# Optimization experiments

Measured on AMD Instinct MI355X. Metric: run time of the kernel, lower is better.

Reference implementation:

```python
import math
import jax, jax.numpy as jnp
import numpy as np

B, S, D, H, V = 8, 1024, 512, 8, 32000
HD = D // H


def _position_embedding(seq_len, d_model):
    pos = jnp.arange(seq_len, dtype=jnp.float32)[:, None]                 # [S,1]
    div = jnp.exp(jnp.arange(0, d_model, 2, dtype=jnp.float32) * (-math.log(10000.0) / d_model))  # [D/2]
    ang = pos * div                                                        # [S,D/2]
    # interleave sin (even cols) / cos (odd cols)
    return jnp.stack([jnp.sin(ang), jnp.cos(ang)], axis=-1).reshape(seq_len, d_model)


def _min_max_normalize(w):
    lo = jnp.min(w, axis=-1, keepdims=True)
    hi = jnp.max(w, axis=-1, keepdims=True)
    return (w - lo) / (hi - lo)


def _converable_mask(h, Wc, bc):
    bs, seq = h.shape[0], h.shape[1]
    half = seq // 2
    shift = math.ceil(seq / 2)
    width = jnp.einsum('bsd,od->bso', h, Wc)[..., 0] + bc[0]               # [B,S]
    width = _min_max_normalize(width)[..., None]                           # [B,S,1]
    origin = jnp.concatenate([jnp.linspace(1.0, 0.0, half),
                              jnp.linspace(0.0, 1.0, seq - half)])         # [S]
    origin_mask = 1.0 - jax.nn.sigmoid((origin[None, None, :] - width) * 100.0)  # [B,S,S]
    idx = (jnp.arange(seq - 1, -1, -1)[:, None] + jnp.arange(seq)[None, :]) % seq  # [S,S]
    idx = jnp.roll(idx, shift, axis=0)
    # torch.roll of a [1,S] row along dim 0 is a no-op
    cmp = idx >= jnp.arange(seq)[None, :]                                  # [S,S] bool
    move = jnp.concatenate([cmp[:shift], ~cmp[shift:]], axis=0)            # [S,S]
    gathered = jnp.take_along_axis(origin_mask, idx[None, :, :], axis=2)   # [B,S,S]
    return gathered * move.astype(origin_mask.dtype)


def setup_inputs():
    key = jax.random.key(0)
    ks = jax.random.split(key, 9)
    s_emb = 1.0
    s_hd = 1.0 / math.sqrt(HD)
    s_d = 1.0 / math.sqrt(D)
    return {
        'x':   jax.random.randint(ks[0], (B, S), 0, V),
        'emb': jax.random.normal(ks[1], (V, D), dtype=jnp.float32) * s_emb,
        'Wq':  jax.random.normal(ks[2], (HD, HD), dtype=jnp.float32) * s_hd,
        'Wk':  jax.random.normal(ks[3], (HD, HD), dtype=jnp.float32) * s_hd,
        'Wv':  jax.random.normal(ks[4], (HD, HD), dtype=jnp.float32) * s_hd,
        'Wo':  jax.random.normal(ks[5], (D, D), dtype=jnp.float32) * s_d,
        'bo':  jnp.zeros((D,), dtype=jnp.float32),
        'Wc':  jax.random.normal(ks[6], (1, D), dtype=jnp.float32) * s_d,
        'bc':  jnp.zeros((1,), dtype=jnp.float32),
    }


def reference(x, emb, Wq, Wk, Wv, Wo, bo, Wc, bc):
    h = emb[x] + _position_embedding(S, D)[None]                           # [B,S,D]
    mask = _converable_mask(h, Wc, bc)                                     # [B,S,S]
    hh = h.reshape(B, S, H, HD)
    q = jnp.einsum('bshd,od->bsho', hh, Wq)
    k = jnp.einsum('bshd,od->bsho', hh, Wk)
    v = jnp.einsum('bshd,od->bsho', hh, Wv)
    energy = jnp.einsum('bqhd,bkhd->bhqk', q, k)                           # [B,H,S,S]
    # mask [B,S,S] broadcasts as [1,B,S,S]; valid because B == H (as in original)
    energy = energy * mask
    attn = jax.nn.softmax(energy / math.sqrt(D), axis=3)
    out = jnp.einsum('bhqk,bkhd->bqhd', attn, v).reshape(B, S, D)
    out = out @ Wo.T + bo
    return (out, mask)
```

## Files before the change

kernel.cpp:

```cpp
#include <hip/hip_runtime.h>
#include <hip/hip_bf16.h>
#include <math.h>

#define Bn 8
#define Sn 1024
#define Dn 512
#define Hn 8
#define HDn 64

typedef __bf16 bf16x8 __attribute__((ext_vector_type(8)));
typedef __bf16 bf16x4 __attribute__((ext_vector_type(4)));
typedef __bf16 bf16x2 __attribute__((ext_vector_type(2)));
typedef float  f32x4  __attribute__((ext_vector_type(4)));
typedef float  f32x16 __attribute__((ext_vector_type(16)));
typedef unsigned int u32x4 __attribute__((ext_vector_type(4)));
typedef int i32x2 __attribute__((ext_vector_type(2)));

__device__ __forceinline__ unsigned enc_f(float v) {
    unsigned u = __float_as_uint(v);
    return (u & 0x80000000u) ? ~u : (u | 0x80000000u);
}
__device__ __forceinline__ float dec_f(unsigned k) {
    unsigned u = (k & 0x80000000u) ? (k ^ 0x80000000u) : ~k;
    return __uint_as_float(u);
}

__global__ __launch_bounds__(256) void k_fused(
        const int* __restrict__ x, const float* __restrict__ emb,
        const float* __restrict__ Wc, const float* __restrict__ bc,
        const float* __restrict__ Wq, const float* __restrict__ Wk,
        const float* __restrict__ Wv,
        float* __restrict__ width, unsigned* __restrict__ lohi,
        __bf16* __restrict__ q, __bf16* __restrict__ k, __bf16* __restrict__ vt) {
    __shared__ __align__(16) __bf16 Xs[64][72];
    __shared__ __align__(16) __bf16 WqS[64][72];
    __shared__ __align__(16) __bf16 WkS[64][72];
    __shared__ __align__(16) __bf16 WvS[64][72];
    __shared__ float wtok[8];
    int t = threadIdx.x;
    int bs0 = blockIdx.x * 8;
    int m0 = blockIdx.x * 64;
    int w = t >> 6, lane = t & 63, quad = lane >> 4, li = lane & 15;

    {
        int token = t >> 5, l32 = t & 31;
        int bs = bs0 + token;
        int s = bs & (Sn - 1);
        int tok = x[bs];
        float wpart = 0.f;
        int row = token * 8 + ((l32 * 16) >> 6);
        #pragma unroll
        for (int j = 0; j < 4; ++j) {
            int d0 = l32 * 16 + j * 4;
            float4 ev = *(const float4*)&emb[(size_t)tok * Dn + d0];
            float4 wc = *(const float4*)&Wc[d0];
            float hv[4];
            #pragma unroll
            for (int i = 0; i < 4; ++i) {
                int d = d0 + i;
                float f = __expf((float)(d & ~1) * (-9.210340371976184f / 512.0f));
                float ang = (float)s * f;
                float pe = (d & 1) ? __cosf(ang) : __sinf(ang);
                hv[i] = (&ev.x)[i] + pe;
                wpart += hv[i] * (&wc.x)[i];
            }
            *(bf16x4*)&Xs[row][d0 & 63] =
                (bf16x4){(__bf16)hv[0], (__bf16)hv[1], (__bf16)hv[2], (__bf16)hv[3]};
        }
        #pragma unroll
        for (int off = 1; off < 32; off <<= 1) wpart += __shfl_xor(wpart, off);
        if (l32 == 0) { float wv = wpart + bc[0]; width[bs] = wv; wtok[token] = wv; }
    }
    #pragma unroll
    for (int it = 0; it < 4; ++it) {
        int e = (it * 256 + t) * 4; int r = e >> 6, c = e & 63;
        float4 qv = *(const float4*)&Wq[e];
        *(bf16x4*)&WqS[r][c] = (bf16x4){(__bf16)qv.x, (__bf16)qv.y, (__bf16)qv.z, (__bf16)qv.w};
        float4 kv = *(const float4*)&Wk[e];
        *(bf16x4*)&WkS[r][c] = (bf16x4){(__bf16)kv.x, (__bf16)kv.y, (__bf16)kv.z, (__bf16)kv.w};
        float4 vv = *(const float4*)&Wv[e];
        *(bf16x4*)&WvS[r][c] = (bf16x4){(__bf16)vv.x, (__bf16)vv.y, (__bf16)vv.z, (__bf16)vv.w};
    }
    __syncthreads();

    if (t == 0) {
        float mn = wtok[0], mx = wtok[0];
        #pragma unroll
        for (int i = 1; i < 8; ++i) { mn = fminf(mn, wtok[i]); mx = fmaxf(mx, wtok[i]); }
        int b = bs0 >> 10;
        atomicMin(&lohi[b], enc_f(mn));
        atomicMin(&lohi[8 + b], ~enc_f(mx));
    }

    bf16x8 A0 = *(const bf16x8*)&Xs[w * 16 + li][quad * 8];
    bf16x8 A1 = *(const bf16x8*)&Xs[w * 16 + li][32 + quad * 8];
    f32x4 aq[4], ak[4], av[4];
    #pragma unroll
    for (int n = 0; n < 4; ++n) {
        aq[n] = (f32x4){0.f,0.f,0.f,0.f}; ak[n] = aq[n]; av[n] = aq[n];
        bf16x8 Bq0 = *(const bf16x8*)&WqS[n * 16 + li][quad * 8];
        bf16x8 Bq1 = *(const bf16x8*)&WqS[n * 16 + li][32 + quad * 8];
        aq[n] = __builtin_amdgcn_mfma_f32_16x16x32_bf16(A0, Bq0, aq[n], 0, 0, 0);
        aq[n] = __builtin_amdgcn_mfma_f32_16x16x32_bf16(A1, Bq1, aq[n], 0, 0, 0);
        bf16x8 Bk0 = *(const bf16x8*)&WkS[n * 16 + li][quad * 8];
        bf16x8 Bk1 = *(const bf16x8*)&WkS[n * 16 + li][32 + quad * 8];
        ak[n] = __builtin_amdgcn_mfma_f32_16x16x32_bf16(A0, Bk0, ak[n], 0, 0, 0);
        ak[n] = __builtin_amdgcn_mfma_f32_16x16x32_bf16(A1, Bk1, ak[n], 0, 0, 0);
        bf16x8 Bv0 = *(const bf16x8*)&WvS[n * 16 + li][quad * 8];
        bf16x8 Bv1 = *(const bf16x8*)&WvS[n * 16 + li][32 + quad * 8];
        av[n] = __builtin_amdgcn_mfma_f32_16x16x32_bf16(A0, Bv0, av[n], 0, 0, 0);
        av[n] = __builtin_amdgcn_mfma_f32_16x16x32_bf16(A1, Bv1, av[n], 0, 0, 0);
    }

    const float SCALE = 0.04419417382415922f;
    __syncthreads();
    #pragma unroll
    for (int n = 0; n < 4; ++n)
        #pragma unroll
        for (int r = 0; r < 4; ++r) {
            int row = w * 16 + quad * 4 + r, col = n * 16 + li;
            WkS[row][col] = (__bf16)(aq[n][r] * SCALE);
            WvS[row][col] = (__bf16)ak[n][r];
            WqS[row][col] = (__bf16)av[n][r];
        }
    __syncthreads();

    {
        int row = t >> 2, part = (t & 3) * 16;
        int Rg = m0 + row;
        int bsI = Rg >> 3, head = Rg & 7;
        int bq = bsI >> 10, sq = bsI & (Sn - 1);
        size_t base = (((size_t)(bq * Hn + head)) * Sn + sq) * HDn + part;
        *(bf16x8*)&q[base]     = *(bf16x8*)&WkS[row][part];
        *(bf16x8*)&q[base + 8] = *(bf16x8*)&WkS[row][part + 8];
        *(bf16x8*)&k[base]     = *(bf16x8*)&WvS[row][part];
        *(bf16x8*)&k[base + 8] = *(bf16x8*)&WvS[row][part + 8];
    }

    __bf16 (*Vs)[72] = WqS;
    int bs0i = m0 >> 3;
    int b = bs0i >> 10, s0l = bs0i & (Sn - 1);
    #pragma unroll
    for (int i = 0; i < 2; ++i) {
        int p = t + 256 * i;
        int head = p >> 6, o = p & 63;
        __bf16 tmp[8];
        #pragma unroll
        for (int j = 0; j < 8; ++j) tmp[j] = Vs[j * 8 + head][o];
        *(bf16x8*)&vt[(((size_t)(b * Hn + head)) * HDn + o) * Sn + s0l] = *(bf16x8*)tmp;
    }
}

__global__ void k_mask(const float* __restrict__ width, const unsigned* __restrict__ lohi,
                       float* __restrict__ mask_out, __bf16* __restrict__ maskb) {
    int bs = blockIdx.x;
    int b = bs >> 10;
    int s = bs & (Sn - 1);
    float lo = dec_f(lohi[b]);
    float hi = dec_f(~lohi[8 + b]);
    float wn = (width[bs] - lo) / (hi - lo);
    for (int t = threadIdx.x; t < Sn; t += 256) {
        int it = (t - s + 1535) & (Sn - 1);
        float origin = (it < 512) ? (1.0f - (float)it * (1.0f / 511.0f))
                                  : ((float)(it - 512) * (1.0f / 511.0f));
        float z = (origin - wn) * 100.0f;
        float om;
        if (z >= 0.0f) { float e = __expf(-z); om = e / (1.0f + e); }
        else           { float e = __expf(z);  om = 1.0f / (1.0f + e); }
        bool cmpv = (it >= t);
        bool mv = (s < 512) ? cmpv : !cmpv;
        float val = mv ? om : 0.0f;
        mask_out[(size_t)bs * Sn + t] = val;
        maskb[(size_t)bs * Sn + t] = (__bf16)val;
    }
}

__global__ __launch_bounds__(256, 2) void k_attn(
        const __bf16* __restrict__ q, const __bf16* __restrict__ k,
        const __bf16* __restrict__ vt, const __bf16* __restrict__ maskb,
        __bf16* __restrict__ ao) {
    __shared__ __align__(16) __bf16 Ks[2][64][72];
    __shared__ __align__(16) __bf16 Vt[2][64][72];
    int blk = blockIdx.x;
    int hh = blk & 7;
    int qt = (blk >> 3) & 7;
    int b  = blk >> 6;
    int bh = b * Hn + hh;
    int q0 = qt * 128;
    int t = threadIdx.x;
    int w = t >> 6, lane = t & 63, hi5 = lane >> 5, l31 = lane & 31;

    const __bf16* qbase  = q  + ((size_t)bh * Sn + q0 + w * 32) * HDn;
    const __bf16* kbase  = k  + (size_t)bh * Sn * HDn;
    const __bf16* vtbase = vt + (size_t)bh * HDn * Sn;
    const __bf16* mq = maskb + ((size_t)hh * Sn + q0 + w * 32 + l31) * Sn;

    bf16x8 Qf[4];
    #pragma unroll
    for (int c = 0; c < 4; ++c)
        Qf[c] = *(const bf16x8*)&qbase[(size_t)l31 * HDn + c * 16 + hi5 * 8];

    int sr0 = t >> 3, sc0 = (t & 7) * 8;
    bf16x8 pk0, pk1, pv0, pv1;
    pk0 = *(const bf16x8*)&kbase[(size_t)sr0 * HDn + sc0];
    pk1 = *(const bf16x8*)&kbase[(size_t)(sr0 + 32) * HDn + sc0];
    pv0 = *(const bf16x8*)&vtbase[(size_t)sr0 * Sn + sc0];
    pv1 = *(const bf16x8*)&vtbase[(size_t)(sr0 + 32) * Sn + sc0];
    *(bf16x8*)&Ks[0][sr0][sc0] = pk0;
    *(bf16x8*)&Ks[0][sr0 + 32][sc0] = pk1;
    *(bf16x8*)&Vt[0][sr0][sc0] = pv0;
    *(bf16x8*)&Vt[0][sr0 + 32][sc0] = pv1;

    bf16x4 mc[2][4];
    #pragma unroll
    for (int kg = 0; kg < 2; ++kg)
        #pragma unroll
        for (int g = 0; g < 4; ++g)
            mc[kg][g] = *(const bf16x4*)&mq[kg * 32 + g * 8 + hi5 * 4];

    __syncthreads();

    f32x16 OT[2];
    OT[0] = (f32x16){0.f,0.f,0.f,0.f,0.f,0.f,0.f,0.f,0.f,0.f,0.f,0.f,0.f,0.f,0.f,0.f};
    OT[1] = OT[0];
    float rs = 0.f;

    for (int ti = 0; ti < 16; ++ti) {
        int cur = ti & 1;

        bf16x4 mn_[2][4];
        if (ti < 15) {
            int k0n = (ti + 1) * 64;
            #pragma unroll
            for (int kg = 0; kg < 2; ++kg)
                #pragma unroll
                for (int g = 0; g < 4; ++g)
                    mn_[kg][g] = *(const bf16x4*)&mq[k0n + kg * 32 + g * 8 + hi5 * 4];
            pk0 = *(const bf16x8*)&kbase[(size_t)(k0n + sr0) * HDn + sc0];
            pk1 = *(const bf16x8*)&kbase[(size_t)(k0n + sr0 + 32) * HDn + sc0];
            pv0 = *(const bf16x8*)&vtbase[(size_t)sr0 * Sn + k0n + sc0];
            pv1 = *(const bf16x8*)&vtbase[(size_t)(sr0 + 32) * Sn + k0n + sc0];
        }

        bf16x8 Kf[2][4], Vf[2][4];
        #pragma unroll
        for (int h = 0; h < 2; ++h)
            #pragma unroll
            for (int c = 0; c < 4; ++c)
                Kf[h][c] = *(const bf16x8*)&Ks[cur][h * 32 + l31][c * 16 + hi5 * 8];
        #pragma unroll
        for (int h = 0; h < 2; ++h)
            #pragma unroll
            for (int c = 0; c < 4; ++c)
                Vf[h][c] = *(const bf16x8*)&Vt[cur][h * 32 + l31][c * 16 + hi5 * 8];

        f32x16 St[2];
        St[0] = (f32x16){0.f,0.f,0.f,0.f,0.f,0.f,0.f,0.f,0.f,0.f,0.f,0.f,0.f,0.f,0.f,0.f};
        St[1] = St[0];
        __builtin_amdgcn_s_setprio(1);
        #pragma unroll
        for (int c = 0; c < 4; ++c) {
            St[0] = __builtin_amdgcn_mfma_f32_32x32x16_bf16(Kf[0][c], Qf[c], St[0], 0, 0, 0);
            St[1] = __builtin_amdgcn_mfma_f32_32x32x16_bf16(Kf[1][c], Qf[c], St[1], 0, 0, 0);
        }
        __builtin_amdgcn_s_setprio(0);

        unsigned pkd[2][4][2];
        #pragma unroll
        for (int kg = 0; kg < 2; ++kg) {
            #pragma unroll
            for (int g = 0; g < 4; ++g) {
                float p0 = __expf(St[kg][4 * g + 0] * (float)mc[kg][g][0]);
                float p1 = __expf(St[kg][4 * g + 1] * (float)mc[kg][g][1]);
                float p2 = __expf(St[kg][4 * g + 2] * (float)mc[kg][g][2]);
                float p3 = __expf(St[kg][4 * g + 3] * (float)mc[kg][g][3]);
                rs += (p0 + p1) + (p2 + p3);
                bf16x2 plo = { (__bf16)p0, (__bf16)p1 };
                bf16x2 phi = { (__bf16)p2, (__bf16)p3 };
                pkd[kg][g][0] = __builtin_bit_cast(unsigned, plo);
                pkd[kg][g][1] = __builtin_bit_cast(unsigned, phi);
            }
        }

        __builtin_amdgcn_s_setprio(1);
        #pragma unroll
        for (int c = 0; c < 4; ++c) {
            const int kg = c >> 1, gA = 2 * (c & 1), gB = gA + 1;
            i32x2 r0 = __builtin_amdgcn_permlane32_swap(
                (int)pkd[kg][gA][0], (int)pkd[kg][gB][0], false, false);
            i32x2 r1 = __builtin_amdgcn_permlane32_swap(
                (int)pkd[kg][gA][1], (int)pkd[kg][gB][1], false, false);
            u32x4 du;
            du[0] = (unsigned)r0[0];
            du[1] = (unsigned)r1[0];
            du[2] = (unsigned)r0[1];
            du[3] = (unsigned)r1[1];
            bf16x8 Pf = __builtin_bit_cast(bf16x8, du);
            OT[0] = __builtin_amdgcn_mfma_f32_32x32x16_bf16(Vf[0][c], Pf, OT[0], 0, 0, 0);
            OT[1] = __builtin_amdgcn_mfma_f32_32x32x16_bf16(Vf[1][c], Pf, OT[1], 0, 0, 0);
        }
        __builtin_amdgcn_s_setprio(0);

        if (ti < 15) {
            *(bf16x8*)&Ks[cur ^ 1][sr0][sc0] = pk0;
            *(bf16x8*)&Ks[cur ^ 1][sr0 + 32][sc0] = pk1;
            *(bf16x8*)&Vt[cur ^ 1][sr0][sc0] = pv0;
            *(bf16x8*)&Vt[cur ^ 1][sr0 + 32][sc0] = pv1;
            __syncthreads();
            #pragma unroll
            for (int kg = 0; kg < 2; ++kg)
                #pragma unroll
                for (int g = 0; g < 4; ++g)
                    mc[kg][g] = mn_[kg][g];
        }
    }

    rs += __shfl_xor(rs, 32);
    float inv = __fdividef(1.0f, rs);

    size_t orow = ((size_t)b * Sn + q0 + w * 32 + l31) * Dn + hh * HDn;
    #pragma unroll
    for (int og = 0; og < 2; ++og)
        #pragma unroll
        for (int g2 = 0; g2 < 4; ++g2) {
            bf16x4 ov = { (__bf16)(OT[og][4 * g2 + 0] * inv),
                          (__bf16)(OT[og][4 * g2 + 1] * inv),
                          (__bf16)(OT[og][4 * g2 + 2] * inv),
                          (__bf16)(OT[og][4 * g2 + 3] * inv) };
            *(bf16x4*)&ao[orow + og * 32 + g2 * 8 + hi5 * 4] = ov;
        }
}

__global__ __launch_bounds__(256) void k_proj(
        const __bf16* __restrict__ ao, const float* __restrict__ Wo,
        const float* __restrict__ bo, float* __restrict__ out) {
    __shared__ __align__(16) __bf16 As[64][72];
    __shared__ __align__(16) __bf16 Bs[64][72];
    __shared__ __align__(16) float  Os[64][68];
    int bm = blockIdx.x >> 3;
    int bn = blockIdx.x & 7;
    int m0 = bm * 64, n0 = bn * 64;
    int t = threadIdx.x;
    int w = t >> 6, lane = t & 63, quad = lane >> 4, li = lane & 15;

    f32x4 O[4];
    #pragma unroll
    for (int n = 0; n < 4; ++n) O[n] = (f32x4){0.f, 0.f, 0.f, 0.f};

    for (int k0 = 0; k0 < Dn; k0 += 64) {
        if (k0) __syncthreads();
        #pragma unroll
        for (int it = 0; it < 2; ++it) {
            int e = (it * 256 + t) * 8; int r = e >> 6, c = e & 63;
            *(bf16x8*)&As[r][c] = *(const bf16x8*)&ao[(size_t)(m0 + r) * Dn + k0 + c];
        }
        #pragma unroll
        for (int it = 0; it < 4; ++it) {
            int e = (it * 256 + t) * 4; int r = e >> 6, c = e & 63;
            float4 wv = *(const float4*)&Wo[(size_t)(n0 + r) * Dn + k0 + c];
            *(bf16x4*)&Bs[r][c] = (bf16x4){(__bf16)wv.x, (__bf16)wv.y, (__bf16)wv.z, (__bf16)wv.w};
        }
        __syncthreads();

        bf16x8 A0 = *(const bf16x8*)&As[w * 16 + li][quad * 8];
        bf16x8 A1 = *(const bf16x8*)&As[w * 16 + li][32 + quad * 8];
        #pragma unroll
        for (int n = 0; n < 4; ++n) {
            bf16x8 B0 = *(const bf16x8*)&Bs[n * 16 + li][quad * 8];
            O[n] = __builtin_amdgcn_mfma_f32_16x16x32_bf16(A0, B0, O[n], 0, 0, 0);
            bf16x8 B1 = *(const bf16x8*)&Bs[n * 16 + li][32 + quad * 8];
            O[n] = __builtin_amdgcn_mfma_f32_16x16x32_bf16(A1, B1, O[n], 0, 0, 0);
        }
    }

    #pragma unroll
    for (int n = 0; n < 4; ++n) {
        float bias = bo[n0 + n * 16 + li];
        #pragma unroll
        for (int r = 0; r < 4; ++r)
            Os[w * 16 + quad * 4 + r][n * 16 + li] = O[n][r] + bias;
    }
    __syncthreads();
    {
        int row = t >> 2, part = (t & 3) * 16;
        size_t base = (size_t)(m0 + row) * Dn + n0 + part;
        #pragma unroll
        for (int j = 0; j < 4; ++j)
            *(float4*)&out[base + j * 4] = *(const float4*)&Os[row][part + j * 4];
    }
}

extern "C" void kernel_launch(void* const* d_in, const int* in_sizes, int n_in,
                              void* d_out, int out_size, void* d_ws, size_t ws_size,
                              hipStream_t stream) {
    const int*   x   = (const int*)d_in[0];
    const float* emb = (const float*)d_in[1];
    const float* Wq  = (const float*)d_in[2];
    const float* Wk  = (const float*)d_in[3];
    const float* Wv  = (const float*)d_in[4];
    const float* Wo  = (const float*)d_in[5];
    const float* bo  = (const float*)d_in[6];
    const float* Wc  = (const float*)d_in[7];
    const float* bc  = (const float*)d_in[8];

    float* ws      = (float*)d_ws;
    float* width   = ws;
    unsigned* lohi = (unsigned*)(width + Bn * Sn);
    __bf16* qb   = (__bf16*)(ws + Bn * Sn + 16);
    __bf16* kb   = qb + (size_t)Bn * Sn * Dn;
    __bf16* vtb  = kb + (size_t)Bn * Sn * Dn;
    __bf16* maskb = vtb + (size_t)Bn * Sn * Dn;
    __bf16* ao   = maskb + (size_t)Bn * Sn * Sn;

    float* out      = (float*)d_out;
    float* mask_out = out + (size_t)Bn * Sn * Dn;

    hipMemsetAsync(lohi, 0xFF, 16 * sizeof(unsigned), stream);
    k_fused<<<(Bn * Sn) / 8, 256, 0, stream>>>(x, emb, Wc, bc, Wq, Wk, Wv,
                                               width, lohi, qb, kb, vtb);
    k_mask<<<Bn * Sn, 256, 0, stream>>>(width, lohi, mask_out, maskb);
    k_attn<<<Bn * Hn * (Sn / 128), 256, 0, stream>>>(qb, kb, vtb, maskb, ao);
    k_proj<<<(Bn * Sn / 64) * (Dn / 64), 256, 0, stream>>>(ao, Wo, bo, out);
}
```

Baseline: 214.3 us.

## Load K/V MFMA fragments directly from global memory, drop LDS staging

The attention kernel stops staging K and V tiles through double-buffered shared memory with block-wide barriers. Each wave now loads its MFMA operand fragments straight from global memory every iteration, and the 16-step key loop is fully unrolled so the compiler can schedule those loads early. This removes the LDS writes, LDS reads and __syncthreads per tile. In exchange, each of the 4 waves reads the same K/V data separately, which relies on L1/L2 hits, and explicit software prefetch of the next tile is lost.

```diff
diff --git a/kernel.cpp b/kernel.cpp
--- a/kernel.cpp
+++ b/kernel.cpp
@@ -179,8 +179,6 @@
         const __bf16* __restrict__ q, const __bf16* __restrict__ k,
         const __bf16* __restrict__ vt, const __bf16* __restrict__ maskb,
         __bf16* __restrict__ ao) {
-    __shared__ __align__(16) __bf16 Ks[2][64][72];
-    __shared__ __align__(16) __bf16 Vt[2][64][72];
     int blk = blockIdx.x;
     int hh = blk & 7;
     int qt = (blk >> 3) & 7;
@@ -190,69 +188,40 @@
     int t = threadIdx.x;
     int w = t >> 6, lane = t & 63, hi5 = lane >> 5, l31 = lane & 31;
 
-    const __bf16* qbase  = q  + ((size_t)bh * Sn + q0 + w * 32) * HDn;
-    const __bf16* kbase  = k  + (size_t)bh * Sn * HDn;
-    const __bf16* vtbase = vt + (size_t)bh * HDn * Sn;
-    const __bf16* mq = maskb + ((size_t)hh * Sn + q0 + w * 32 + l31) * Sn;
+    const __bf16* qbase = q  + ((size_t)bh * Sn + q0 + w * 32) * HDn;
+    const __bf16* kfrag = k  + (size_t)bh * Sn * HDn + (size_t)l31 * HDn + hi5 * 8;
+    const __bf16* vfrag = vt + (size_t)bh * HDn * Sn + (size_t)l31 * Sn + hi5 * 8;
+    const __bf16* mq = maskb + ((size_t)hh * Sn + q0 + w * 32 + l31) * Sn + hi5 * 4;
 
     bf16x8 Qf[4];
     #pragma unroll
     for (int c = 0; c < 4; ++c)
         Qf[c] = *(const bf16x8*)&qbase[(size_t)l31 * HDn + c * 16 + hi5 * 8];
-
-    int sr0 = t >> 3, sc0 = (t & 7) * 8;
-    bf16x8 pk0, pk1, pv0, pv1;
-    pk0 = *(const bf16x8*)&kbase[(size_t)sr0 * HDn + sc0];
-    pk1 = *(const bf16x8*)&kbase[(size_t)(sr0 + 32) * HDn + sc0];
-    pv0 = *(const bf16x8*)&vtbase[(size_t)sr0 * Sn + sc0];
-    pv1 = *(const bf16x8*)&vtbase[(size_t)(sr0 + 32) * Sn + sc0];
-    *(bf16x8*)&Ks[0][sr0][sc0] = pk0;
-    *(bf16x8*)&Ks[0][sr0 + 32][sc0] = pk1;
-    *(bf16x8*)&Vt[0][sr0][sc0] = pv0;
-    *(bf16x8*)&Vt[0][sr0 + 32][sc0] = pv1;
-
-    bf16x4 mc[2][4];
-    #pragma unroll
-    for (int kg = 0; kg < 2; ++kg)
-        #pragma unroll
-        for (int g = 0; g < 4; ++g)
-            mc[kg][g] = *(const bf16x4*)&mq[kg * 32 + g * 8 + hi5 * 4];
-
-    __syncthreads();
 
     f32x16 OT[2];
     OT[0] = (f32x16){0.f,0.f,0.f,0.f,0.f,0.f,0.f,0.f,0.f,0.f,0.f,0.f,0.f,0.f,0.f,0.f};
     OT[1] = OT[0];
     float rs = 0.f;
 
+    #pragma unroll
     for (int ti = 0; ti < 16; ++ti) {
-        int cur = ti & 1;
-
-        bf16x4 mn_[2][4];
-        if (ti < 15) {
-            int k0n = (ti + 1) * 64;
+        const int k0 = ti * 64;
+
+        bf16x4 mcv[2][4];
+        #pragma unroll
+        for (int kg = 0; kg < 2; ++kg)
             #pragma unroll
-            for (int kg = 0; kg < 2; ++kg)
-                #pragma unroll
-                for (int g = 0; g < 4; ++g)
-                    mn_[kg][g] = *(const bf16x4*)&mq[k0n + kg * 32 + g * 8 + hi5 * 4];
-            pk0 = *(const bf16x8*)&kbase[(size_t)(k0n + sr0) * HDn + sc0];
-            pk1 = *(const bf16x8*)&kbase[(size_t)(k0n + sr0 + 32) * HDn + sc0];
-            pv0 = *(const bf16x8*)&vtbase[(size_t)sr0 * Sn + k0n + sc0];
-            pv1 = *(const bf16x8*)&vtbase[(size_t)(sr0 + 32) * Sn + k0n + sc0];
-        }
+            for (int g = 0; g < 4; ++g)
+                mcv[kg][g] = *(const bf16x4*)&mq[k0 + kg * 32 + g * 8];
 
         bf16x8 Kf[2][4], Vf[2][4];
         #pragma unroll
         for (int h = 0; h < 2; ++h)
             #pragma unroll
-            for (int c = 0; c < 4; ++c)
-                Kf[h][c] = *(const bf16x8*)&Ks[cur][h * 32 + l31][c * 16 + hi5 * 8];
-        #pragma unroll
-        for (int h = 0; h < 2; ++h)
-            #pragma unroll
-            for (int c = 0; c < 4; ++c)
-                Vf[h][c] = *(const bf16x8*)&Vt[cur][h * 32 + l31][c * 16 + hi5 * 8];
+            for (int c = 0; c < 4; ++c) {
+                Kf[h][c] = *(const bf16x8*)&kfrag[(size_t)(k0 + h * 32) * HDn + c * 16];
+                Vf[h][c] = *(const bf16x8*)&vfrag[(size_t)(h * 32) * Sn + k0 + c * 16];
+            }
 
         f32x16 St[2];
         St[0] = (f32x16){0.f,0.f,0.f,0.f,0.f,0.f,0.f,0.f,0.f,0.f,0.f,0.f,0.f,0.f,0.f,0.f};
@@ -270,10 +239,10 @@
         for (int kg = 0; kg < 2; ++kg) {
             #pragma unroll
             for (int g = 0; g < 4; ++g) {
-                float p0 = __expf(St[kg][4 * g + 0] * (float)mc[kg][g][0]);
-                float p1 = __expf(St[kg][4 * g + 1] * (float)mc[kg][g][1]);
-                float p2 = __expf(St[kg][4 * g + 2] * (float)mc[kg][g][2]);
-                float p3 = __expf(St[kg][4 * g + 3] * (float)mc[kg][g][3]);
+                float p0 = __expf(St[kg][4 * g + 0] * (float)mcv[kg][g][0]);
+                float p1 = __expf(St[kg][4 * g + 1] * (float)mcv[kg][g][1]);
+                float p2 = __expf(St[kg][4 * g + 2] * (float)mcv[kg][g][2]);
+                float p3 = __expf(St[kg][4 * g + 3] * (float)mcv[kg][g][3]);
                 rs += (p0 + p1) + (p2 + p3);
                 bf16x2 plo = { (__bf16)p0, (__bf16)p1 };
                 bf16x2 phi = { (__bf16)p2, (__bf16)p3 };
@@ -300,19 +269,6 @@
             OT[1] = __builtin_amdgcn_mfma_f32_32x32x16_bf16(Vf[1][c], Pf, OT[1], 0, 0, 0);
         }
         __builtin_amdgcn_s_setprio(0);
-
-        if (ti < 15) {
-            *(bf16x8*)&Ks[cur ^ 1][sr0][sc0] = pk0;
-            *(bf16x8*)&Ks[cur ^ 1][sr0 + 32][sc0] = pk1;
-            *(bf16x8*)&Vt[cur ^ 1][sr0][sc0] = pv0;
-            *(bf16x8*)&Vt[cur ^ 1][sr0 + 32][sc0] = pv1;
-            __syncthreads();
-            #pragma unroll
-            for (int kg = 0; kg < 2; ++kg)
-                #pragma unroll
-                for (int g = 0; g < 4; ++g)
-                    mc[kg][g] = mn_[kg][g];
-        }
     }
 
     rs += __shfl_xor(rs, 32);
```

New measurement: 260.2 us. +21.4%, slower.
